# Kernel tuning notes

Hardware: AMD Instinct MI355X
Metric: run time of the kernel (lower is better)

The kernel has to match this reference:

```python
import jax, jax.numpy as jnp
import numpy as np

EPS = 1e-7


def _softsplat(ten_in, ten_flow):
    # Forward bilinear splatting (scatter-add), faithful to softsplat_func.
    # ten_in: [B,C,H,W], ten_flow: [B,2,H,W] (flow[:,0]=dx, flow[:,1]=dy)
    B, C, H, W = ten_in.shape
    dt = ten_in.dtype
    gx = jnp.arange(W, dtype=dt)
    gy = jnp.arange(H, dtype=dt)
    fx = gx[None, None, :] + ten_flow[:, 0]  # [B,H,W] target x
    fy = gy[None, :, None] + ten_flow[:, 1]  # [B,H,W] target y
    x0 = jnp.floor(fx)
    y0 = jnp.floor(fy)
    x0i = x0.astype(jnp.int32)
    y0i = y0.astype(jnp.int32)
    x1i = x0i + 1
    y1i = y0i + 1
    wx1 = fx - x0  # weight toward x1
    wx0 = 1.0 - wx1
    wy1 = fy - y0
    wy0 = 1.0 - wy1
    # values as [B*H*W, C] rows to scatter
    vals = jnp.transpose(ten_in, (0, 2, 3, 1)).reshape(B * H * W, C)
    boff = jnp.arange(B, dtype=jnp.int32)[:, None, None] * (H * W)  # batch offsets
    out = jnp.zeros((B * H * W, C), dtype=dt)
    corners = ((x0i, y0i, wx0 * wy0), (x1i, y0i, wx1 * wy0),
               (x0i, y1i, wx0 * wy1), (x1i, y1i, wx1 * wy1))
    for xi, yi, w in corners:
        valid = (xi >= 0) & (xi < W) & (yi >= 0) & (yi < H)
        idx = (boff + jnp.clip(yi, 0, H - 1) * W + jnp.clip(xi, 0, W - 1)).reshape(-1)
        wv = jnp.where(valid, w, jnp.zeros_like(w)).reshape(-1, 1)
        out = out.at[idx].add(vals * wv)
    return jnp.transpose(out.reshape(B, H, W, C), (0, 3, 1, 2))


def reference(ten_in, ten_flow, ten_metric):
    # warp(..., strMode='soft'): softmax-style splatting with exp(metric) weights
    m = jnp.exp(ten_metric)                       # [B,1,H,W]
    cat = jnp.concatenate([ten_in * m, m], axis=1)  # [B,C+1,H,W]
    out = _softsplat(cat, ten_flow)
    norm = out[:, -1:, :, :] + EPS                # 'addeps' default branch
    return out[:, :-1, :, :] / norm


def setup_inputs() -> dict:
    key = jax.random.key(0)
    k1, k2, k3 = jax.random.split(key, 3)
    B, C, H, W = 4, 16, 512, 960
    ten_in = jax.random.normal(k1, (B, C, H, W), dtype=jnp.float32)
    # scale flow so splatting is genuinely irregular (multi-pixel displacements)
    ten_flow = jax.random.normal(k2, (B, 2, H, W), dtype=jnp.float32) * 10.0
    ten_metric = jax.random.normal(k3, (B, 1, H, W), dtype=jnp.float32)
    return {"ten_in": ten_in, "ten_flow": ten_flow, "ten_metric": ten_metric}
```

## Files before the change

### kernel.cpp

```cpp
#include <hip/hip_runtime.h>
#include <math.h>


#define BB 4
#define CC 16
#define HH 512
#define WW 960
#define HWP (HH * WW)
#define EPSF 1e-7f

#define NSX 30
#define NSY 256
#define SPB (NSX * NSY)
#define CAPS 192

#define WS_BINS_OFF ((size_t)131072)
#define WS_INT_OFF  (WS_BINS_OFF + (size_t)SPB * CAPS * 16)
#define WS_NEED5    (WS_INT_OFF + (size_t)HWP * 64)

#define TSX 32
#define TSY 16
#define TNX (WW / TSX)
#define TNY (HH / TSY)
#define TPB (TNX * TNY)
#define NTILE (BB * TPB)
#define CAP 1536


__launch_bounds__(256)
__global__ void prep5(const float* __restrict__ in,
                      const float* __restrict__ flow,
                      const float* __restrict__ metric,
                      unsigned int* __restrict__ counts,
                      uint4* __restrict__ bins,
                      float4* __restrict__ inT, int b)
{
    __shared__ unsigned int lcnt[SPB];

    int x = blockIdx.x * 32 + (threadIdx.x & 31);
    int y = blockIdx.y * 8  + (threadIdx.x >> 5);
    int p = y * WW + x;

    for (int i = threadIdx.x; i < SPB; i += 256) lcnt[i] = 0;
    __syncthreads();

    float dx = flow[(size_t)(b * 2 + 0) * HWP + p];
    float dy = flow[(size_t)(b * 2 + 1) * HWP + p];
    float m  = expf(metric[(size_t)b * HWP + p]);

    const float* ib = in + (size_t)b * CC * HWP + p;
    float4* o = inT + (size_t)p * 4;
#pragma unroll
    for (int k = 0; k < 4; ++k) {
        float4 r;
        r.x = ib[(size_t)(4 * k + 0) * HWP];
        r.y = ib[(size_t)(4 * k + 1) * HWP];
        r.z = ib[(size_t)(4 * k + 2) * HWP];
        r.w = ib[(size_t)(4 * k + 3) * HWP];
        o[k] = r;
    }

    float fx = (float)x + dx, fy = (float)y + dy;
    float x0f = floorf(fx),   y0f = floorf(fy);
    int   x0 = (int)x0f,      y0 = (int)y0f;
    float wx1 = fx - x0f,     wy1 = fy - y0f;
    float wy0m = (1.0f - wy1) * m, wy1m = wy1 * m;

    int sxA = x0 >> 5, sxB = (x0 + 1) >> 5;
    int syA = y0 >> 1, syB = (y0 + 1) >> 1;
    bool dupX = (sxB != sxA);
    bool dupY = (syB != syA);

    float w0AB = dupY ? 0.0f  : wy0m;
    float w1AB = dupY ? wy0m  : wy1m;
    float w0CD = wy1m;

    bool vA = (sxA >= 0 && sxA < NSX && syA >= 0 && syA < NSY);
    bool vB = dupX && (sxB >= 0 && sxB < NSX && syA >= 0 && syA < NSY);
    bool vC = dupY && (sxA >= 0 && sxA < NSX && syB >= 0 && syB < NSY);
    bool vD = dupX && dupY && (sxB >= 0 && sxB < NSX && syB >= 0 && syB < NSY);

    int tA = syA * NSX + sxA, tB = syA * NSX + sxB;
    int tC = syB * NSX + sxA, tD = syB * NSX + sxB;

    unsigned int rA = 0, rB = 0, rC = 0, rD = 0;
    if (vA) rA = atomicAdd(&lcnt[tA], 1u);
    if (vB) rB = atomicAdd(&lcnt[tB], 1u);
    if (vC) rC = atomicAdd(&lcnt[tC], 1u);
    if (vD) rD = atomicAdd(&lcnt[tD], 1u);

    __syncthreads();

    for (int i = threadIdx.x; i < SPB; i += 256) {
        unsigned int c = lcnt[i];
        if (c) lcnt[i] = atomicAdd(&counts[i], c);
    }
    __syncthreads();

    unsigned int pkA = (unsigned int)p | ((unsigned int)((x0 - (sxA << 5)) + 1) << 19);
    unsigned int pkB = (unsigned int)p;
    unsigned int uwx = __float_as_uint(wx1);

    if (vA) { unsigned int pos = lcnt[tA] + rA;
        if (pos < CAPS) bins[(size_t)tA * CAPS + pos] =
            make_uint4(pkA, uwx, __float_as_uint(w0AB), __float_as_uint(w1AB)); }
    if (vB) { unsigned int pos = lcnt[tB] + rB;
        if (pos < CAPS) bins[(size_t)tB * CAPS + pos] =
            make_uint4(pkB, uwx, __float_as_uint(w0AB), __float_as_uint(w1AB)); }
    if (vC) { unsigned int pos = lcnt[tC] + rC;
        if (pos < CAPS) bins[(size_t)tC * CAPS + pos] =
            make_uint4(pkA, uwx, __float_as_uint(w0CD), __float_as_uint(0.0f)); }
    if (vD) { unsigned int pos = lcnt[tD] + rD;
        if (pos < CAPS) bins[(size_t)tD * CAPS + pos] =
            make_uint4(pkB, uwx, __float_as_uint(w0CD), __float_as_uint(0.0f)); }
}

__launch_bounds__(256)
__global__ void splat5(const float4* __restrict__ inT,
                       const unsigned int* __restrict__ counts,
                       const uint4* __restrict__ bins,
                       float* __restrict__ out, int b)
{
    int wave = threadIdx.x >> 6;
    int lane = threadIdx.x & 63;
    int bx   = blockIdx.x;
    int sy   = blockIdx.y * 4 + wave;
    int s = __builtin_amdgcn_readfirstlane(sy * NSX + bx);

    unsigned int n = counts[s];
    if (n > CAPS) n = CAPS;
    const uint4* bs = bins + (size_t)s * CAPS;

    int lx = lane & 31;
    int ly = lane >> 5;

    float4 A = make_float4(0.f,0.f,0.f,0.f), B = A, C = A, D = A;
    float  aw = 0.f;

#pragma unroll 2
    for (unsigned int j = 0; j < n; ++j) {
        uint4 e = bs[j];
        int   p   = (int)(e.x & 0x7FFFFu);
        int   cx  = (int)((e.x >> 19) & 63u) - 1;
        float wx1 = __uint_as_float(e.y);
        float wrm = __uint_as_float(ly ? e.w : e.z);
        float wx  = (lx == cx) ? (1.0f - wx1)
                  : ((lx == cx + 1) ? wx1 : 0.0f);
        float w   = wx * wrm;

        const float4* r = inT + (size_t)p * 4;
        float4 t0 = r[0], t1 = r[1], t2 = r[2], t3 = r[3];
        A.x += w * t0.x; A.y += w * t0.y; A.z += w * t0.z; A.w += w * t0.w;
        B.x += w * t1.x; B.y += w * t1.y; B.z += w * t1.z; B.w += w * t1.w;
        C.x += w * t2.x; C.y += w * t2.y; C.z += w * t2.z; C.w += w * t2.w;
        D.x += w * t3.x; D.y += w * t3.y; D.z += w * t3.z; D.w += w * t3.w;
        aw  += w;
    }

    float inv = 1.0f / (aw + EPSF);
    int xg = bx * 32 + lx;
    int yg = sy * 2 + ly;
    float* ob = out + (size_t)b * CC * HWP + (size_t)yg * WW + xg;
    ob[(size_t) 0 * HWP] = A.x * inv;  ob[(size_t) 1 * HWP] = A.y * inv;
    ob[(size_t) 2 * HWP] = A.z * inv;  ob[(size_t) 3 * HWP] = A.w * inv;
    ob[(size_t) 4 * HWP] = B.x * inv;  ob[(size_t) 5 * HWP] = B.y * inv;
    ob[(size_t) 6 * HWP] = B.z * inv;  ob[(size_t) 7 * HWP] = B.w * inv;
    ob[(size_t) 8 * HWP] = C.x * inv;  ob[(size_t) 9 * HWP] = C.y * inv;
    ob[(size_t)10 * HWP] = C.z * inv;  ob[(size_t)11 * HWP] = C.w * inv;
    ob[(size_t)12 * HWP] = D.x * inv;  ob[(size_t)13 * HWP] = D.y * inv;
    ob[(size_t)14 * HWP] = D.z * inv;  ob[(size_t)15 * HWP] = D.w * inv;
}


__launch_bounds__(256)
__global__ void bin_kernel(const float* __restrict__ flow,
                           unsigned int* __restrict__ counts,
                           unsigned int* __restrict__ bins)
{
    __shared__ unsigned int lcnt[TPB];

    int b  = blockIdx.z;
    int x  = blockIdx.x * 32 + (threadIdx.x & 31);
    int y  = blockIdx.y * 8  + (threadIdx.x >> 5);
    int p  = y * WW + x;

    for (int i = threadIdx.x; i < TPB; i += 256) lcnt[i] = 0;
    __syncthreads();

    float dx = flow[(size_t)(b * 2 + 0) * HWP + p];
    float dy = flow[(size_t)(b * 2 + 1) * HWP + p];
    int x0 = (int)floorf((float)x + dx);
    int y0 = (int)floorf((float)y + dy);

    int txA = x0 >> 5, txB = (x0 + 1) >> 5;
    int tyA = y0 >> 4, tyB = (y0 + 1) >> 4;

    int          tA[4];
    unsigned int rA[4];
    int cnt = 0;

    #define TRYINS(tx_, ty_)                                                   \
        if ((tx_) >= 0 && (tx_) < TNX && (ty_) >= 0 && (ty_) < TNY) {          \
            int t_ = (ty_) * TNX + (tx_);                                      \
            rA[cnt] = atomicAdd(&lcnt[t_], 1u);                                \
            tA[cnt] = t_;                                                      \
            ++cnt;                                                             \
        }

    TRYINS(txA, tyA);
    if (txB != txA) TRYINS(txB, tyA);
    if (tyB != tyA) {
        TRYINS(txA, tyB);
        if (txB != txA) TRYINS(txB, tyB);
    }
    #undef TRYINS

    __syncthreads();

    for (int i = threadIdx.x; i < TPB; i += 256) {
        unsigned int c = lcnt[i];
        if (c) lcnt[i] = atomicAdd(&counts[b * TPB + i], c);
    }
    __syncthreads();

    unsigned int e = ((unsigned int)y << 10) | (unsigned int)x;
    for (int k = 0; k < cnt; ++k) {
        int t_ = tA[k];
        unsigned int pos = lcnt[t_] + rA[k];
        if (pos < CAP)
            bins[((size_t)(b * TPB) + t_) * CAP + pos] = e;
    }
}

__launch_bounds__(256)
__global__ void tile_kernel(const float* __restrict__ in,
                            const float* __restrict__ flow,
                            const float* __restrict__ metric,
                            const unsigned int* __restrict__ counts,
                            const unsigned int* __restrict__ bins,
                            float* __restrict__ out)
{
    __shared__ float acc[TSX * TSY * 17];

    int tile = blockIdx.x;
    int b  = tile / TPB;
    int t  = tile - b * TPB;
    int ty = t / TNX;
    int tx = t - ty * TNX;
    int tid = threadIdx.x;

    for (int i = tid; i < TSX * TSY * 17; i += 256) acc[i] = 0.0f;
    __syncthreads();

    unsigned int n = counts[tile];
    if (n > CAP) n = CAP;

    for (unsigned int base = 0; base < n; base += 256) {
        unsigned int i = base + tid;
        if (i < n) {
            unsigned int e = bins[(size_t)tile * CAP + i];
            int x = (int)(e & 1023u);
            int y = (int)(e >> 10);
            int p = y * WW + x;

            float dx = flow[(size_t)(b * 2 + 0) * HWP + p];
            float dy = flow[(size_t)(b * 2 + 1) * HWP + p];
            float m  = expf(metric[(size_t)b * HWP + p]);

            float fx = (float)x + dx;
            float fy = (float)y + dy;
            float x0f = floorf(fx), y0f = floorf(fy);
            int   x0  = (int)x0f,   y0  = (int)y0f;
            float wx1 = fx - x0f,   wy1 = fy - y0f;
            float wx0 = 1.0f - wx1, wy0 = 1.0f - wy1;

            float v[CC];
            const float* inp = in + (size_t)b * CC * HWP + p;
#pragma unroll
            for (int c = 0; c < CC; ++c) v[c] = inp[(size_t)c * HWP] * m;

            const int   xs[4] = { x0,        x0 + 1,    x0,        x0 + 1    };
            const int   ys[4] = { y0,        y0,        y0 + 1,    y0 + 1    };
            const float ws[4] = { wx0 * wy0, wx1 * wy0, wx0 * wy1, wx1 * wy1 };

#pragma unroll
            for (int k = 0; k < 4; ++k) {
                int xi = xs[k], yi = ys[k];
                if ((xi >> 5) == tx && (yi >> 4) == ty) {
                    float wgt = ws[k];
                    int q = ((yi & 15) * TSX + (xi & 31)) * 17;
#pragma unroll
                    for (int c = 0; c < CC; ++c)
                        atomicAdd(&acc[q + c], v[c] * wgt);
                    atomicAdd(&acc[q + CC], m * wgt);
                }
            }
        }
    }
    __syncthreads();

    for (int q = tid; q < TSX * TSY; q += 256) {
        int ly = q >> 5, lx = q & 31;
        int gp = (ty * TSY + ly) * WW + tx * TSX + lx;
        float inv = 1.0f / (acc[q * 17 + CC] + EPSF);
        float* op = out + (size_t)b * CC * HWP + gp;
#pragma unroll
        for (int c = 0; c < CC; ++c)
            op[(size_t)c * HWP] = acc[q * 17 + c] * inv;
    }
}


extern "C" void kernel_launch(void* const* d_in, const int* in_sizes, int n_in,
                              void* d_out, int out_size, void* d_ws, size_t ws_size,
                              hipStream_t stream) {
    const float* in     = (const float*)d_in[0];
    const float* flow   = (const float*)d_in[1];
    const float* metric = (const float*)d_in[2];
    float* out = (float*)d_out;

    if (ws_size >= WS_NEED5) {
        unsigned int* counts = (unsigned int*)d_ws;
        uint4*        bins   = (uint4*)((char*)d_ws + WS_BINS_OFF);
        float4*       inT    = (float4*)((char*)d_ws + WS_INT_OFF);

        hipMemsetAsync(counts, 0, (size_t)BB * SPB * 4, stream);

        for (int b = 0; b < BB; ++b) {
            prep5 <<<dim3(NSX, 64), dim3(256), 0, stream>>>(
                in, flow, metric, counts + (size_t)b * SPB, bins, inT, b);
            splat5<<<dim3(NSX, 64), dim3(256), 0, stream>>>(
                inT, counts + (size_t)b * SPB, bins, out, b);
        }
    } else {
        unsigned int* counts = (unsigned int*)d_ws;
        unsigned int* bins   = (unsigned int*)((char*)d_ws + 16384);

        hipMemsetAsync(counts, 0, NTILE * sizeof(unsigned int), stream);

        bin_kernel<<<dim3(WW / 32, HH / 8, BB), dim3(256), 0, stream>>>(flow, counts, bins);
        tile_kernel<<<dim3(NTILE), dim3(256), 0, stream>>>(in, flow, metric, counts, bins, out);
    }
}
```

Before: 479.1 us.

## Batch all images into single prep/splat launches and software-pipeline bin entry loads

Replaces the per-batch loop of eight launches with two launches that cover all four images through blockIdx.z. This requires per-batch copies of the bins and transposed input in workspace. The splat loop now processes two entries per iteration and prefetches the next pair of bin entries while the current input rows load, to hide gather latency. The cost is a much larger workspace requirement: if the workspace is too small, execution falls back to the slower tile path.

After: 508.9 us. 6.2% more time.

```diff
diff --git a/kernel.cpp b/kernel.cpp
--- a/kernel.cpp
+++ b/kernel.cpp
@@ -15,8 +15,8 @@
 #define CAPS 192
 
 #define WS_BINS_OFF ((size_t)131072)
-#define WS_INT_OFF  (WS_BINS_OFF + (size_t)SPB * CAPS * 16)
-#define WS_NEED5    (WS_INT_OFF + (size_t)HWP * 64)
+#define WS_INT_OFF  (WS_BINS_OFF + (size_t)BB * SPB * CAPS * 16)
+#define WS_NEED6    (WS_INT_OFF + (size_t)BB * HWP * 64)
 
 #define TSX 32
 #define TSY 16
@@ -28,19 +28,23 @@
 
 
 __launch_bounds__(256)
-__global__ void prep5(const float* __restrict__ in,
+__global__ void prep6(const float* __restrict__ in,
                       const float* __restrict__ flow,
                       const float* __restrict__ metric,
                       unsigned int* __restrict__ counts,
                       uint4* __restrict__ bins,
-                      float4* __restrict__ inT, int b)
+                      float4* __restrict__ inT)
 {
     __shared__ unsigned int lcnt[SPB];
 
+    int b = blockIdx.z;
     int x = blockIdx.x * 32 + (threadIdx.x & 31);
     int y = blockIdx.y * 8  + (threadIdx.x >> 5);
     int p = y * WW + x;
 
+    unsigned int* cb = counts + (size_t)b * SPB;
+    uint4*        bb = bins   + (size_t)b * SPB * CAPS;
+
     for (int i = threadIdx.x; i < SPB; i += 256) lcnt[i] = 0;
     __syncthreads();
 
@@ -49,7 +53,7 @@
     float m  = expf(metric[(size_t)b * HWP + p]);
 
     const float* ib = in + (size_t)b * CC * HWP + p;
-    float4* o = inT + (size_t)p * 4;
+    float4* o = inT + ((size_t)b * HWP + p) * 4;
 #pragma unroll
     for (int k = 0; k < 4; ++k) {
         float4 r;
@@ -93,7 +97,7 @@
 
     for (int i = threadIdx.x; i < SPB; i += 256) {
         unsigned int c = lcnt[i];
-        if (c) lcnt[i] = atomicAdd(&counts[i], c);
+        if (c) lcnt[i] = atomicAdd(&cb[i], c);
     }
     __syncthreads();
 
@@ -102,34 +106,36 @@
     unsigned int uwx = __float_as_uint(wx1);
 
     if (vA) { unsigned int pos = lcnt[tA] + rA;
-        if (pos < CAPS) bins[(size_t)tA * CAPS + pos] =
+        if (pos < CAPS) bb[(size_t)tA * CAPS + pos] =
             make_uint4(pkA, uwx, __float_as_uint(w0AB), __float_as_uint(w1AB)); }
     if (vB) { unsigned int pos = lcnt[tB] + rB;
-        if (pos < CAPS) bins[(size_t)tB * CAPS + pos] =
+        if (pos < CAPS) bb[(size_t)tB * CAPS + pos] =
             make_uint4(pkB, uwx, __float_as_uint(w0AB), __float_as_uint(w1AB)); }
     if (vC) { unsigned int pos = lcnt[tC] + rC;
-        if (pos < CAPS) bins[(size_t)tC * CAPS + pos] =
+        if (pos < CAPS) bb[(size_t)tC * CAPS + pos] =
             make_uint4(pkA, uwx, __float_as_uint(w0CD), __float_as_uint(0.0f)); }
     if (vD) { unsigned int pos = lcnt[tD] + rD;
-        if (pos < CAPS) bins[(size_t)tD * CAPS + pos] =
+        if (pos < CAPS) bb[(size_t)tD * CAPS + pos] =
             make_uint4(pkB, uwx, __float_as_uint(w0CD), __float_as_uint(0.0f)); }
 }
 
 __launch_bounds__(256)
-__global__ void splat5(const float4* __restrict__ inT,
+__global__ void splat6(const float4* __restrict__ inT,
                        const unsigned int* __restrict__ counts,
                        const uint4* __restrict__ bins,
-                       float* __restrict__ out, int b)
+                       float* __restrict__ out)
 {
     int wave = threadIdx.x >> 6;
     int lane = threadIdx.x & 63;
+    int b    = blockIdx.z;
     int bx   = blockIdx.x;
     int sy   = blockIdx.y * 4 + wave;
     int s = __builtin_amdgcn_readfirstlane(sy * NSX + bx);
 
-    unsigned int n = counts[s];
+    unsigned int n = counts[(size_t)b * SPB + s];
     if (n > CAPS) n = CAPS;
-    const uint4* bs = bins + (size_t)s * CAPS;
+    const uint4*  bs  = bins + ((size_t)b * SPB + s) * CAPS;
+    const float4* ibT = inT + (size_t)b * HWP * 4;
 
     int lx = lane & 31;
     int ly = lane >> 5;
@@ -137,25 +143,37 @@
     float4 A = make_float4(0.f,0.f,0.f,0.f), B = A, C = A, D = A;
     float  aw = 0.f;
 
-#pragma unroll 2
-    for (unsigned int j = 0; j < n; ++j) {
-        uint4 e = bs[j];
-        int   p   = (int)(e.x & 0x7FFFFu);
-        int   cx  = (int)((e.x >> 19) & 63u) - 1;
-        float wx1 = __uint_as_float(e.y);
-        float wrm = __uint_as_float(ly ? e.w : e.z);
-        float wx  = (lx == cx) ? (1.0f - wx1)
-                  : ((lx == cx + 1) ? wx1 : 0.0f);
-        float w   = wx * wrm;
-
-        const float4* r = inT + (size_t)p * 4;
-        float4 t0 = r[0], t1 = r[1], t2 = r[2], t3 = r[3];
-        A.x += w * t0.x; A.y += w * t0.y; A.z += w * t0.z; A.w += w * t0.w;
-        B.x += w * t1.x; B.y += w * t1.y; B.z += w * t1.z; B.w += w * t1.w;
-        C.x += w * t2.x; C.y += w * t2.y; C.z += w * t2.z; C.w += w * t2.w;
-        D.x += w * t3.x; D.y += w * t3.y; D.z += w * t3.z; D.w += w * t3.w;
-        aw  += w;
-    }
+    #define LOADE(idx) (((unsigned int)(idx) < n) ? bs[idx] \
+                                                  : make_uint4(0u,0u,0u,0u))
+
+    #define DOFMA(eK, t0, t1, t2, t3)                                          \
+        {                                                                      \
+            int   cx  = (int)((eK.x >> 19) & 63u) - 1;                         \
+            float wx1 = __uint_as_float(eK.y);                                 \
+            float wrm = __uint_as_float(ly ? eK.w : eK.z);                     \
+            float wx  = (lx == cx) ? (1.0f - wx1)                              \
+                      : ((lx == cx + 1) ? wx1 : 0.0f);                         \
+            float w   = wx * wrm;                                              \
+            A.x += w*t0.x; A.y += w*t0.y; A.z += w*t0.z; A.w += w*t0.w;        \
+            B.x += w*t1.x; B.y += w*t1.y; B.z += w*t1.z; B.w += w*t1.w;        \
+            C.x += w*t2.x; C.y += w*t2.y; C.z += w*t2.z; C.w += w*t2.w;        \
+            D.x += w*t3.x; D.y += w*t3.y; D.z += w*t3.z; D.w += w*t3.w;        \
+            aw  += w;                                                          \
+        }
+
+    uint4 e0 = LOADE(0), e1 = LOADE(1);
+    for (unsigned int j = 0; j < n; j += 2) {
+        const float4* r0 = ibT + (size_t)(e0.x & 0x7FFFFu) * 4;
+        const float4* r1 = ibT + (size_t)(e1.x & 0x7FFFFu) * 4;
+        float4 t00 = r0[0], t01 = r0[1], t02 = r0[2], t03 = r0[3];
+        float4 t10 = r1[0], t11 = r1[1], t12 = r1[2], t13 = r1[3];
+        uint4 f0 = LOADE(j + 2), f1 = LOADE(j + 3);
+        DOFMA(e0, t00, t01, t02, t03)
+        DOFMA(e1, t10, t11, t12, t13)
+        e0 = f0; e1 = f1;
+    }
+    #undef DOFMA
+    #undef LOADE
 
     float inv = 1.0f / (aw + EPSF);
     int xg = bx * 32 + lx;
@@ -319,19 +337,17 @@
     const float* metric = (const float*)d_in[2];
     float* out = (float*)d_out;
 
-    if (ws_size >= WS_NEED5) {
+    if (ws_size >= WS_NEED6) {
         unsigned int* counts = (unsigned int*)d_ws;
         uint4*        bins   = (uint4*)((char*)d_ws + WS_BINS_OFF);
         float4*       inT    = (float4*)((char*)d_ws + WS_INT_OFF);
 
         hipMemsetAsync(counts, 0, (size_t)BB * SPB * 4, stream);
 
-        for (int b = 0; b < BB; ++b) {
-            prep5 <<<dim3(NSX, 64), dim3(256), 0, stream>>>(
-                in, flow, metric, counts + (size_t)b * SPB, bins, inT, b);
-            splat5<<<dim3(NSX, 64), dim3(256), 0, stream>>>(
-                inT, counts + (size_t)b * SPB, bins, out, b);
-        }
+        prep6 <<<dim3(NSX, 64, BB), dim3(256), 0, stream>>>(
+            in, flow, metric, counts, bins, inT);
+        splat6<<<dim3(NSX, 64, BB), dim3(256), 0, stream>>>(
+            inT, counts, bins, out);
     } else {
         unsigned int* counts = (unsigned int*)d_ws;
         unsigned int* bins   = (unsigned int*)((char*)d_ws + 16384);
```
